# Kernel optimization log

Measured on AMD Instinct MI355X. Metric: run time of the kernel, lower is better.

Reference implementation:

```python
import jax, jax.numpy as jnp
import numpy as np

LORA_SCALING = 1.0 / 4.0  # lora_alpha / lora_rank
NUM_HEADS = 16
HEAD_DIM = 64
ROPE_BASE = 20000.0


def rotate_half(x):
    x1, x2 = jnp.split(x, 2, axis=-1)
    return jnp.concatenate([-x2, x1], axis=-1)


def setup_inputs() -> dict:
    key = jax.random.key(0)
    ks = jax.random.split(key, 8)
    B, S, D = 8, 1024, 1024
    hidden_states = jax.random.normal(ks[0], (B, S, D), jnp.float32)
    attention_mask = jnp.zeros((B, 1, 1, S), jnp.float32)
    # real rotary tables (HF style: duplicated half-dim freqs)
    inv_freq = 1.0 / (ROPE_BASE ** (jnp.arange(0, HEAD_DIM, 2, dtype=jnp.float32) / HEAD_DIM))
    t = jnp.arange(S, dtype=jnp.float32)
    freqs = jnp.outer(t, inv_freq)                      # [S, hd/2]
    emb = jnp.concatenate([freqs, freqs], axis=-1)      # [S, hd]
    cos = jnp.broadcast_to(jnp.cos(emb)[None], (B, S, HEAD_DIM))
    sin = jnp.broadcast_to(jnp.sin(emb)[None], (B, S, HEAD_DIM))
    adapter_mask = jax.random.randint(ks[1], (B,), 0, 5, jnp.int32)
    Wqkv_weight = jax.random.normal(ks[2], (3 * D, D), jnp.float32) * 0.02
    Wqkv_bias = jax.random.normal(ks[3], (3 * D,), jnp.float32) * 0.02
    lora_A = jax.random.normal(ks[4], (5, 4, D), jnp.float32) * 0.02
    lora_B = jax.random.normal(ks[5], (5, 3 * D, 4), jnp.float32) * 0.02
    return dict(hidden_states=hidden_states, attention_mask=attention_mask,
                cos=cos, sin=sin, adapter_mask=adapter_mask,
                Wqkv_weight=Wqkv_weight, Wqkv_bias=Wqkv_bias,
                lora_A=lora_A, lora_B=lora_B)


def reference(hidden_states, attention_mask, cos, sin, adapter_mask,
              Wqkv_weight, Wqkv_bias, lora_A, lora_B):
    B, S, D = hidden_states.shape
    H, hd = NUM_HEADS, HEAD_DIM
    # fused QKV projection with per-task LoRA (gather adapters per batch row)
    base = jnp.einsum('bsd,od->bso', hidden_states, Wqkv_weight) + Wqkv_bias
    A_t = lora_A[adapter_mask]                    # [B, r, D]
    B_t = lora_B[adapter_mask]                    # [B, 3D, r]
    lo = jnp.einsum('bsd,brd->bsr', hidden_states, A_t)
    delta = jnp.einsum('bsr,bor->bso', lo, B_t) * LORA_SCALING
    qkv = (base + delta).reshape(B, S, 3, H, hd)
    q = qkv[:, :, 0].transpose(0, 2, 1, 3)        # [B,H,S,hd]
    k = qkv[:, :, 1].transpose(0, 2, 1, 3)
    v = qkv[:, :, 2].transpose(0, 2, 1, 3)
    # inline RoPE
    c = cos[:, None, :, :]
    s = sin[:, None, :, :]
    q = q * c + rotate_half(q) * s
    k = k * c + rotate_half(k) * s
    # eager SDPA
    scaling = hd ** -0.5
    scores = jnp.einsum('bhqd,bhkd->bhqk', q, k) * scaling + attention_mask
    attn = jax.nn.softmax(scores, axis=-1)
    out = jnp.einsum('bhqk,bhkd->bhqd', attn, v)
    return out.transpose(0, 2, 1, 3).reshape(B, S, H * hd)
```

## Files before the change

### kernel.cpp

```cpp
#include <hip/hip_runtime.h>
#include <hip/hip_bf16.h>
#include <stdint.h>

typedef __attribute__((ext_vector_type(8))) short short8;
typedef __attribute__((ext_vector_type(4))) float f32x4;
typedef unsigned short ushort_t;

#define MFMA16(a, b, c) __builtin_amdgcn_mfma_f32_16x16x32_bf16((a), (b), (c), 0, 0, 0)
#define EXP2F(x) __builtin_amdgcn_exp2f(x)
#define BAR() __builtin_amdgcn_s_barrier()


__device__ __forceinline__ float bf2f(unsigned short u) {
    union { unsigned int i; float f; } x; x.i = ((unsigned int)u) << 16; return x.f;
}
__device__ __forceinline__ unsigned short f2bf(float f) {
    union { float f; unsigned int i; } x; x.f = f;
    unsigned int i = x.i;
    i = i + 0x7FFFu + ((i >> 16) & 1u);
    return (unsigned short)(i >> 16);
}
__device__ __forceinline__ unsigned int pack2(float a, float b) {
    return (unsigned int)f2bf(a) | ((unsigned int)f2bf(b) << 16);
}
__device__ __forceinline__ void glds16(const void* gsrc, void* ldst) {
    __builtin_amdgcn_global_load_lds(
        (const __attribute__((address_space(1))) unsigned int*)gsrc,
        (__attribute__((address_space(3))) unsigned int*)ldst, 16, 0, 0);
}

__global__ __launch_bounds__(256) void prep_kernel(
    const float* __restrict__ hidden,
    const float* __restrict__ W,
    const float* __restrict__ loraA,
    const int* __restrict__ adapter_mask,
    ushort_t* __restrict__ Hb,
    ushort_t* __restrict__ Wb,
    float4* __restrict__ lo)
{
    int tid = threadIdx.x;
    int wave = tid >> 6, lane = tid & 63;
    int row = blockIdx.x * 4 + wave;
    if (row < 8192) {
        int b = row >> 10;
        int a = adapter_mask[b];
        const float4* hp = (const float4*)(hidden + (size_t)row * 1024);
        float4 hv[4];
#pragma unroll
        for (int c = 0; c < 4; ++c) hv[c] = hp[c * 64 + lane];
#pragma unroll
        for (int c = 0; c < 4; ++c) {
            uint2 pk;
            pk.x = pack2(hv[c].x, hv[c].y);
            pk.y = pack2(hv[c].z, hv[c].w);
            *(uint2*)(Hb + (size_t)row * 1024 + c * 256 + lane * 4) = pk;
        }
        const float4* Ap = (const float4*)(loraA + (size_t)a * 4096);
        float acc[4];
#pragma unroll
        for (int r = 0; r < 4; ++r) {
            float s = 0.f;
#pragma unroll
            for (int c = 0; c < 4; ++c) {
                float4 av = Ap[r * 64 + c * 16 + (lane >> 2) * 1 + 0];
                s += 0.f * av.x;
            }
            acc[r] = s;
        }
#pragma unroll
        for (int r = 0; r < 4; ++r) {
            float s = 0.f;
#pragma unroll
            for (int c = 0; c < 4; ++c) {
                float4 av = Ap[(size_t)r * 256 + c * 64 + lane];
                s += hv[c].x * av.x + hv[c].y * av.y + hv[c].z * av.z + hv[c].w * av.w;
            }
            acc[r] = s;
        }
        for (int off = 32; off > 0; off >>= 1)
#pragma unroll
            for (int r = 0; r < 4; ++r) acc[r] += __shfl_xor(acc[r], off);
        if (lane == 0) lo[row] = make_float4(acc[0], acc[1], acc[2], acc[3]);
    } else {
        int rw = row - 8192;
        const float4* wp = (const float4*)(W + (size_t)rw * 1024);
        float4 wv[4];
#pragma unroll
        for (int c = 0; c < 4; ++c) wv[c] = wp[c * 64 + lane];
#pragma unroll
        for (int c = 0; c < 4; ++c) {
            uint2 pk;
            pk.x = pack2(wv[c].x, wv[c].y);
            pk.y = pack2(wv[c].z, wv[c].w);
            *(uint2*)(Wb + (size_t)rw * 1024 + c * 256 + lane * 4) = pk;
        }
    }
}

__global__ __launch_bounds__(512, 2) void qkv_gemm_kernel(
    const ushort_t* __restrict__ Hb,
    const ushort_t* __restrict__ Wb,
    const float* __restrict__ bias,
    const float4* __restrict__ lo,
    const float* __restrict__ loraB,
    const int* __restrict__ adapter_mask,
    const float* __restrict__ cosp,
    const float* __restrict__ sinp,
    ushort_t* __restrict__ qw,
    ushort_t* __restrict__ kw,
    ushort_t* __restrict__ vt)
{
    __shared__ __align__(16) ushort_t As[2][16384];
    __shared__ __align__(16) ushort_t Bs[2][16384];
    int tid = threadIdx.x;
    int wave = tid >> 6, lane = tid & 63, quad = lane >> 4, l16 = lane & 15;
    int wm = wave >> 2, wn = wave & 3;

    int wg = (blockIdx.x & 7) * 48 + (blockIdx.x >> 3);
    int bx = wg % 12, by = wg / 12;
    int n0 = bx * 256;
    int m0 = by * 256;

    int r_ = tid >> 3, c_ = (tid & 7) ^ (r_ & 7);
    const ushort_t* pA0 = Hb + (size_t)(m0 +   0 + r_) * 1024 + c_ * 8;
    const ushort_t* pA1 = Hb + (size_t)(m0 +  64 + r_) * 1024 + c_ * 8;
    const ushort_t* pA2 = Hb + (size_t)(m0 + 128 + r_) * 1024 + c_ * 8;
    const ushort_t* pA3 = Hb + (size_t)(m0 + 192 + r_) * 1024 + c_ * 8;
    const ushort_t* pB0 = Wb + (size_t)(n0 +   0 + r_) * 1024 + c_ * 8;
    const ushort_t* pB1 = Wb + (size_t)(n0 +  64 + r_) * 1024 + c_ * 8;
    const ushort_t* pB2 = Wb + (size_t)(n0 + 128 + r_) * 1024 + c_ * 8;
    const ushort_t* pB3 = Wb + (size_t)(n0 + 192 + r_) * 1024 + c_ * 8;
    char* stA0 = (char*)&As[0][0] + wave * 1024;
    char* stB0 = (char*)&Bs[0][0] + wave * 1024;

    f32x4 acc[8][4];
#pragma unroll
    for (int i = 0; i < 8; ++i)
#pragma unroll
        for (int j = 0; j < 4; ++j) acc[i][j] = (f32x4)0.f;

    glds16(pB0, stB0);          glds16(pB1, stB0 + 8192);
    glds16(pB2, stB0 + 16384);  glds16(pB3, stB0 + 24576);
    glds16(pA0, stA0);          glds16(pA1, stA0 + 8192);
    glds16(pA2, stA0 + 16384);  glds16(pA3, stA0 + 24576);
    glds16(pB0 + 64, stB0 + 32768);          glds16(pB1 + 64, stB0 + 32768 + 8192);
    glds16(pB2 + 64, stB0 + 32768 + 16384);  glds16(pB3 + 64, stB0 + 32768 + 24576);

#pragma unroll 2
    for (int t = 0; t < 16; ++t) {
        int cur = t & 1;
        const char* rdA = (const char*)&As[0][0] + cur * 32768;
        const char* rdB = (const char*)&Bs[0][0] + cur * 32768;
        char* sA = stA0 + (cur ^ 1) * 32768;
        char* sB = stB0 + cur * 32768;
        int kA = (t + 1) << 6;
        int kB = (t + 2) << 6;

        if (t < 15) { asm volatile("s_waitcnt vmcnt(4)" ::: "memory"); }
        else        { asm volatile("s_waitcnt vmcnt(0)" ::: "memory"); }
        BAR();
        if (t < 15) {
            glds16(pA0 + kA, sA);          glds16(pA1 + kA, sA + 8192);
            glds16(pA2 + kA, sA + 16384);  glds16(pA3 + kA, sA + 24576);
        }
        short8 bfr[4][2];
#pragma unroll
        for (int ni = 0; ni < 4; ++ni) {
            int rb = ni * 16 + l16;
            bfr[ni][0] = *(const short8*)(rdB + wn * 8192 + (rb * 8 + ((quad    ) ^ (rb & 7))) * 16);
            bfr[ni][1] = *(const short8*)(rdB + wn * 8192 + (rb * 8 + ((quad + 4) ^ (rb & 7))) * 16);
        }
        asm volatile("s_waitcnt lgkmcnt(0)" ::: "memory");
        BAR();
        if (t < 14) {
            glds16(pB0 + kB, sB);          glds16(pB1 + kB, sB + 8192);
            glds16(pB2 + kB, sB + 16384);  glds16(pB3 + kB, sB + 24576);
        }
        __builtin_amdgcn_s_setprio(1);
#pragma unroll
        for (int mi = 0; mi < 8; ++mi) {
            int u = wm * 2 + (mi >> 2);
            int rr = (mi & 3) * 16 + l16;
            short8 a0 = *(const short8*)(rdA + u * 8192 + (rr * 8 + ((quad    ) ^ (rr & 7))) * 16);
            short8 a1 = *(const short8*)(rdA + u * 8192 + (rr * 8 + ((quad + 4) ^ (rr & 7))) * 16);
            acc[mi][0] = MFMA16(a0, bfr[0][0], acc[mi][0]);
            acc[mi][1] = MFMA16(a0, bfr[1][0], acc[mi][1]);
            acc[mi][2] = MFMA16(a0, bfr[2][0], acc[mi][2]);
            acc[mi][3] = MFMA16(a0, bfr[3][0], acc[mi][3]);
            acc[mi][0] = MFMA16(a1, bfr[0][1], acc[mi][0]);
            acc[mi][1] = MFMA16(a1, bfr[1][1], acc[mi][1]);
            acc[mi][2] = MFMA16(a1, bfr[2][1], acc[mi][2]);
            acc[mi][3] = MFMA16(a1, bfr[3][1], acc[mi][3]);
        }
        __builtin_amdgcn_s_setprio(0);
    }

    int t_qkv = n0 >> 10;
    int b = m0 >> 10;
    int a_idx = adapter_mask[b];
    float bi[4], bb[4][4];
    int cpos[4], chh[4];
#pragma unroll
    for (int ni = 0; ni < 4; ++ni) {
        int c = n0 + wn * 64 + ni * 16 + l16;
        bi[ni] = bias[c];
        const float* Bp = loraB + ((size_t)a_idx * 3072 + c) * 4;
        bb[ni][0] = Bp[0]; bb[ni][1] = Bp[1]; bb[ni][2] = Bp[2]; bb[ni][3] = Bp[3];
        cpos[ni] = c & 63; chh[ni] = (c >> 6) & 15;
    }
#pragma unroll
    for (int mi = 0; mi < 8; ++mi) {
        float vals[4][4];
        int mrow0 = m0 + wm * 128 + mi * 16 + quad * 4;
#pragma unroll
        for (int r = 0; r < 4; ++r) {
            float4 lov = lo[mrow0 + r];
#pragma unroll
            for (int ni = 0; ni < 4; ++ni)
                vals[r][ni] = acc[mi][ni][r] + bi[ni]
                      + 0.25f * (lov.x * bb[ni][0] + lov.y * bb[ni][1]
                               + lov.z * bb[ni][2] + lov.w * bb[ni][3]);
        }
        int s0 = mrow0 & 1023;
        if (t_qkv < 2) {
#pragma unroll
            for (int r = 0; r < 4; ++r) {
                int s = s0 + r;
                size_t cb = ((size_t)b * 1024 + s) * 64;
                float cA = cosp[cb + l16],      sA_ = sinp[cb + l16];
                float cB = cosp[cb + 16 + l16], sB_ = sinp[cb + 16 + l16];
                float w0 = vals[r][0] * cA - vals[r][2] * sA_;
                float w2 = vals[r][2] * cA + vals[r][0] * sA_;
                float w1 = vals[r][1] * cB - vals[r][3] * sB_;
                float w3 = vals[r][3] * cB + vals[r][1] * sB_;
                float v[4] = {w0, w1, w2, w3};
#pragma unroll
                for (int ni = 0; ni < 4; ++ni) {
                    size_t bh = (size_t)b * 16 + chh[ni];
                    ushort_t ob = f2bf(v[ni]);
                    if (t_qkv == 0) qw[(bh * 1024 + s) * 64 + cpos[ni]] = ob;
                    else            kw[(bh * 1024 + s) * 64 + cpos[ni]] = ob;
                }
            }
        } else {
#pragma unroll
            for (int ni = 0; ni < 4; ++ni) {
                uint2 pk;
                pk.x = pack2(vals[0][ni], vals[1][ni]);
                pk.y = pack2(vals[2][ni], vals[3][ni]);
                size_t bh = (size_t)b * 16 + chh[ni];
                *(uint2*)&vt[(bh * 64 + cpos[ni]) * 1024 + s0] = pk;
            }
        }
    }
}

__global__ __launch_bounds__(256) void attn_kernel(
    const ushort_t* __restrict__ qw,
    const ushort_t* __restrict__ kw,
    const ushort_t* __restrict__ vt,
    const float* __restrict__ mask,
    float* __restrict__ out)
{
    __shared__ __align__(16) ushort_t Kt[3][4096];
    __shared__ __align__(16) ushort_t Vt[3][4096];
    __shared__ __align__(16) ushort_t Ps[4][32][72];
    __shared__ float mlds[1024];
    const float KSCALE = 0.125f * 1.44269504f;
    int tid = threadIdx.x;
    int wave = tid >> 6, lane = tid & 63, quad = lane >> 4, l16 = lane & 15;
    int id = blockIdx.x;
    int qt = id >> 7;
    int bh = id & 127;
    int b = bh >> 4, h = bh & 15;
    size_t base = (size_t)bh * 65536;
    int q0 = qt * 128 + wave * 32;

    for (int i = tid; i < 1024; i += 256) mlds[i] = mask[b * 1024 + i] * 1.44269504f;

    const ushort_t* kbase = kw + base;
    const ushort_t* vbase = vt + base;

    int n0 = tid, n1 = tid + 256;
    int r0 = n0 >> 3, c0 = (n0 & 7) ^ (r0 & 7);
    int r1 = n1 >> 3, c1 = (n1 & 7) ^ (r1 & 7);

    short8 qf[2][2];
    for (int mt = 0; mt < 2; ++mt)
        for (int kt = 0; kt < 2; ++kt)
            qf[mt][kt] = *(const short8*)(qw + base + (size_t)(q0 + mt * 16 + l16) * 64 + kt * 32 + quad * 8);

    f32x4 oacc[2][4], sum_acc[2];
    for (int mt = 0; mt < 2; ++mt) {
        sum_acc[mt] = (f32x4)0.f;
        for (int nt = 0; nt < 4; ++nt) oacc[mt][nt] = (f32x4)0.f;
    }

    short8 ones;
    for (int j = 0; j < 8; ++j) ones[j] = (short)0x3F80;

    __syncthreads();

    int koff[4][2], voff[4][2];
    for (int nt = 0; nt < 4; ++nt)
        for (int kt = 0; kt < 2; ++kt) {
            int rr = nt * 16 + l16;
            int cc = (kt * 4 + quad) ^ (rr & 7);
            koff[nt][kt] = (rr * 8 + cc) * 8;
            voff[nt][kt] = (rr * 8 + cc) * 8;
        }

    {
        char* kd = (char*)&Kt[0][0] + wave * 1024;
        char* vd = (char*)&Vt[0][0] + wave * 1024;
        glds16(kbase + (size_t)r0 * 64 + c0 * 8, kd);
        glds16(kbase + (size_t)r1 * 64 + c1 * 8, kd + 4096);
        glds16(vbase + (size_t)r0 * 1024 + c0 * 8, vd);
        glds16(vbase + (size_t)r1 * 1024 + c1 * 8, vd + 4096);
        kd = (char*)&Kt[1][0] + wave * 1024;
        vd = (char*)&Vt[1][0] + wave * 1024;
        glds16(kbase + (size_t)(64 + r0) * 64 + c0 * 8, kd);
        glds16(kbase + (size_t)(64 + r1) * 64 + c1 * 8, kd + 4096);
        glds16(vbase + (size_t)r0 * 1024 + 64 + c0 * 8, vd);
        glds16(vbase + (size_t)r1 * 1024 + 64 + c1 * 8, vd + 4096);
    }

    const ushort_t* kR  = &Kt[0][0];  const ushort_t* vR  = &Vt[0][0];
    const ushort_t* kN1 = &Kt[1][0];  const ushort_t* vN1 = &Vt[1][0];
    const ushort_t* kN2 = &Kt[2][0];  const ushort_t* vN2 = &Vt[2][0];

    for (int it = 0; it < 16; ++it) {
        int kt0 = it * 64;
        if (it < 15) { asm volatile("s_waitcnt vmcnt(4)" ::: "memory"); }
        else         { asm volatile("s_waitcnt vmcnt(0)" ::: "memory"); }
        BAR();
        __builtin_amdgcn_sched_barrier(0);
        if (it < 14) {
            int kn = kt0 + 128;
            char* kd = (char*)kN2 + wave * 1024;
            char* vd = (char*)vN2 + wave * 1024;
            glds16(kbase + (size_t)(kn + r0) * 64 + c0 * 8, kd);
            glds16(kbase + (size_t)(kn + r1) * 64 + c1 * 8, kd + 4096);
            glds16(vbase + (size_t)r0 * 1024 + kn + c0 * 8, vd);
            glds16(vbase + (size_t)r1 * 1024 + kn + c1 * 8, vd + 4096);
        }
        short8 kf[4][2];
        for (int nt = 0; nt < 4; ++nt)
            for (int kt = 0; kt < 2; ++kt)
                kf[nt][kt] = *(const short8*)&kR[koff[nt][kt]];
        f32x4 sacc[2][4];
        for (int mt = 0; mt < 2; ++mt)
            for (int nt = 0; nt < 4; ++nt) {
                f32x4 z = (f32x4)0.f;
                z = MFMA16(qf[mt][0], kf[nt][0], z);
                z = MFMA16(qf[mt][1], kf[nt][1], z);
                sacc[mt][nt] = z;
            }
        float mv[4];
        for (int nt = 0; nt < 4; ++nt) mv[nt] = mlds[kt0 + nt * 16 + l16];
        for (int mt = 0; mt < 2; ++mt)
            for (int nt = 0; nt < 4; ++nt)
                for (int r = 0; r < 4; ++r) {
                    float p = EXP2F(sacc[mt][nt][r] * KSCALE + mv[nt]);
                    Ps[wave][mt * 16 + quad * 4 + r][nt * 16 + l16] = f2bf(p);
                }
        short8 pf[2][2];
        for (int mt = 0; mt < 2; ++mt)
            for (int kt = 0; kt < 2; ++kt)
                pf[mt][kt] = *(const short8*)&Ps[wave][mt * 16 + l16][kt * 32 + quad * 8];
        short8 vf[4][2];
        for (int nt = 0; nt < 4; ++nt)
            for (int kt = 0; kt < 2; ++kt)
                vf[nt][kt] = *(const short8*)&vR[voff[nt][kt]];
        for (int mt = 0; mt < 2; ++mt) {
            for (int nt = 0; nt < 4; ++nt) {
                oacc[mt][nt] = MFMA16(pf[mt][0], vf[nt][0], oacc[mt][nt]);
                oacc[mt][nt] = MFMA16(pf[mt][1], vf[nt][1], oacc[mt][nt]);
            }
            sum_acc[mt] = MFMA16(pf[mt][0], ones, sum_acc[mt]);
            sum_acc[mt] = MFMA16(pf[mt][1], ones, sum_acc[mt]);
        }
        const ushort_t* tk = kR; kR = kN1; kN1 = kN2; kN2 = tk;
        const ushort_t* tv = vR; vR = vN1; vN1 = vN2; vN2 = tv;
    }

    for (int mt = 0; mt < 2; ++mt) {
        for (int r = 0; r < 4; ++r) {
            float inv = 1.f / sum_acc[mt][r];
            int s = q0 + mt * 16 + quad * 4 + r;
            size_t ob = ((size_t)b * 1024 + s) * 1024 + h * 64;
            for (int nt = 0; nt < 4; ++nt)
                out[ob + nt * 16 + l16] = oacc[mt][nt][r] * inv;
        }
    }
}

extern "C" void kernel_launch(void* const* d_in, const int* in_sizes, int n_in,
                              void* d_out, int out_size, void* d_ws, size_t ws_size,
                              hipStream_t stream)
{
    const float* hidden = (const float*)d_in[0];
    const float* mask   = (const float*)d_in[1];
    const float* cosp   = (const float*)d_in[2];
    const float* sinp   = (const float*)d_in[3];
    const int* adapter_mask = (const int*)d_in[4];
    const float* W      = (const float*)d_in[5];
    const float* bias   = (const float*)d_in[6];
    const float* loraA  = (const float*)d_in[7];
    const float* loraB  = (const float*)d_in[8];
    float* out = (float*)d_out;

    char* ws = (char*)d_ws;
    float4* lo = (float4*)ws;
    ushort_t* qw = (ushort_t*)(ws + (1 << 20));
    ushort_t* kw = qw + (size_t)8 * 16 * 1024 * 64;
    ushort_t* vt = kw + (size_t)8 * 16 * 1024 * 64;

    ushort_t* Hb = (ushort_t*)d_out;
    ushort_t* Wb = Hb + (size_t)8192 * 1024;

    prep_kernel<<<2816, 256, 0, stream>>>(hidden, W, loraA, adapter_mask, Hb, Wb, lo);
    qkv_gemm_kernel<<<384, 512, 0, stream>>>(Hb, Wb, bias, lo, loraB, adapter_mask,
                                             cosp, sinp, qw, kw, vt);
    attn_kernel<<<1024, 256, 0, stream>>>(qw, kw, vt, mask, out);
}
```

Measured before the change: 245.9 us.

## Process two query tiles per attention block to reuse staged K/V tiles

```diff
diff --git a/kernel.cpp b/kernel.cpp
--- a/kernel.cpp
+++ b/kernel.cpp
@@ -57,16 +57,6 @@
         }
         const float4* Ap = (const float4*)(loraA + (size_t)a * 4096);
         float acc[4];
-#pragma unroll
-        for (int r = 0; r < 4; ++r) {
-            float s = 0.f;
-#pragma unroll
-            for (int c = 0; c < 4; ++c) {
-                float4 av = Ap[r * 64 + c * 16 + (lane >> 2) * 1 + 0];
-                s += 0.f * av.x;
-            }
-            acc[r] = s;
-        }
 #pragma unroll
         for (int r = 0; r < 4; ++r) {
             float s = 0.f;
@@ -255,7 +245,7 @@
     }
 }
 
-__global__ __launch_bounds__(256) void attn_kernel(
+__global__ __launch_bounds__(256, 2) void attn_kernel(
     const ushort_t* __restrict__ qw,
     const ushort_t* __restrict__ kw,
     const ushort_t* __restrict__ vt,
@@ -270,11 +260,11 @@
     int tid = threadIdx.x;
     int wave = tid >> 6, lane = tid & 63, quad = lane >> 4, l16 = lane & 15;
     int id = blockIdx.x;
-    int qt = id >> 7;
+    int qp = id >> 7;
     int bh = id & 127;
     int b = bh >> 4, h = bh & 15;
     size_t base = (size_t)bh * 65536;
-    int q0 = qt * 128 + wave * 32;
+    int q0 = qp * 256 + wave * 32;
 
     for (int i = tid; i < 1024; i += 256) mlds[i] = mask[b * 1024 + i] * 1.44269504f;
 
@@ -285,13 +275,15 @@
     int r0 = n0 >> 3, c0 = (n0 & 7) ^ (r0 & 7);
     int r1 = n1 >> 3, c1 = (n1 & 7) ^ (r1 & 7);
 
-    short8 qf[2][2];
-    for (int mt = 0; mt < 2; ++mt)
+    short8 qf[4][2];
+    for (int mt = 0; mt < 4; ++mt) {
+        int qr = q0 + (mt >> 1) * 128 + (mt & 1) * 16;
         for (int kt = 0; kt < 2; ++kt)
-            qf[mt][kt] = *(const short8*)(qw + base + (size_t)(q0 + mt * 16 + l16) * 64 + kt * 32 + quad * 8);
-
-    f32x4 oacc[2][4], sum_acc[2];
-    for (int mt = 0; mt < 2; ++mt) {
+            qf[mt][kt] = *(const short8*)(qw + base + (size_t)(qr + l16) * 64 + kt * 32 + quad * 8);
+    }
+
+    f32x4 oacc[4][4], sum_acc[4];
+    for (int mt = 0; mt < 4; ++mt) {
         sum_acc[mt] = (f32x4)0.f;
         for (int nt = 0; nt < 4; ++nt) oacc[mt][nt] = (f32x4)0.f;
     }
@@ -344,50 +336,71 @@
             glds16(vbase + (size_t)r0 * 1024 + kn + c0 * 8, vd);
             glds16(vbase + (size_t)r1 * 1024 + kn + c1 * 8, vd + 4096);
         }
-        short8 kf[4][2];
-        for (int nt = 0; nt < 4; ++nt)
-            for (int kt = 0; kt < 2; ++kt)
-                kf[nt][kt] = *(const short8*)&kR[koff[nt][kt]];
-        f32x4 sacc[2][4];
-        for (int mt = 0; mt < 2; ++mt)
-            for (int nt = 0; nt < 4; ++nt) {
-                f32x4 z = (f32x4)0.f;
-                z = MFMA16(qf[mt][0], kf[nt][0], z);
-                z = MFMA16(qf[mt][1], kf[nt][1], z);
-                sacc[mt][nt] = z;
-            }
         float mv[4];
         for (int nt = 0; nt < 4; ++nt) mv[nt] = mlds[kt0 + nt * 16 + l16];
-        for (int mt = 0; mt < 2; ++mt)
-            for (int nt = 0; nt < 4; ++nt)
-                for (int r = 0; r < 4; ++r) {
-                    float p = EXP2F(sacc[mt][nt][r] * KSCALE + mv[nt]);
-                    Ps[wave][mt * 16 + quad * 4 + r][nt * 16 + l16] = f2bf(p);
+
+#pragma unroll
+        for (int ph = 0; ph < 2; ++ph) {
+            f32x4 sacc[2][4];
+            {
+                short8 kf[4][2];
+#pragma unroll
+                for (int nt = 0; nt < 4; ++nt)
+#pragma unroll
+                    for (int kt = 0; kt < 2; ++kt)
+                        kf[nt][kt] = *(const short8*)&kR[koff[nt][kt]];
+#pragma unroll
+                for (int mt = 0; mt < 2; ++mt)
+#pragma unroll
+                    for (int nt = 0; nt < 4; ++nt) {
+                        f32x4 z = (f32x4)0.f;
+                        z = MFMA16(qf[ph * 2 + mt][0], kf[nt][0], z);
+                        z = MFMA16(qf[ph * 2 + mt][1], kf[nt][1], z);
+                        sacc[mt][nt] = z;
+                    }
+            }
+#pragma unroll
+            for (int mt = 0; mt < 2; ++mt)
+#pragma unroll
+                for (int nt = 0; nt < 4; ++nt)
+#pragma unroll
+                    for (int r = 0; r < 4; ++r) {
+                        float p = EXP2F(sacc[mt][nt][r] * KSCALE + mv[nt]);
+                        Ps[wave][mt * 16 + quad * 4 + r][nt * 16 + l16] = f2bf(p);
+                    }
+            short8 pf[2][2];
+#pragma unroll
+            for (int mt = 0; mt < 2; ++mt)
+#pragma unroll
+                for (int kt = 0; kt < 2; ++kt)
+                    pf[mt][kt] = *(const short8*)&Ps[wave][mt * 16 + l16][kt * 32 + quad * 8];
+            {
+                short8 vf[4][2];
+#pragma unroll
+                for (int nt = 0; nt < 4; ++nt)
+#pragma unroll
+                    for (int kt = 0; kt < 2; ++kt)
+                        vf[nt][kt] = *(const short8*)&vR[voff[nt][kt]];
+#pragma unroll
+                for (int mt = 0; mt < 2; ++mt) {
+#pragma unroll
+                    for (int nt = 0; nt < 4; ++nt) {
+                        oacc[ph * 2 + mt][nt] = MFMA16(pf[mt][0], vf[nt][0], oacc[ph * 2 + mt][nt]);
+                        oacc[ph * 2 + mt][nt] = MFMA16(pf[mt][1], vf[nt][1], oacc[ph * 2 + mt][nt]);
+                    }
+                    sum_acc[ph * 2 + mt] = MFMA16(pf[mt][0], ones, sum_acc[ph * 2 + mt]);
+                    sum_acc[ph * 2 + mt] = MFMA16(pf[mt][1], ones, sum_acc[ph * 2 + mt]);
                 }
-        short8 pf[2][2];
-        for (int mt = 0; mt < 2; ++mt)
-            for (int kt = 0; kt < 2; ++kt)
-                pf[mt][kt] = *(const short8*)&Ps[wave][mt * 16 + l16][kt * 32 + quad * 8];
-        short8 vf[4][2];
-        for (int nt = 0; nt < 4; ++nt)
-            for (int kt = 0; kt < 2; ++kt)
-                vf[nt][kt] = *(const short8*)&vR[voff[nt][kt]];
-        for (int mt = 0; mt < 2; ++mt) {
-            for (int nt = 0; nt < 4; ++nt) {
-                oacc[mt][nt] = MFMA16(pf[mt][0], vf[nt][0], oacc[mt][nt]);
-                oacc[mt][nt] = MFMA16(pf[mt][1], vf[nt][1], oacc[mt][nt]);
             }
-            sum_acc[mt] = MFMA16(pf[mt][0], ones, sum_acc[mt]);
-            sum_acc[mt] = MFMA16(pf[mt][1], ones, sum_acc[mt]);
         }
         const ushort_t* tk = kR; kR = kN1; kN1 = kN2; kN2 = tk;
         const ushort_t* tv = vR; vR = vN1; vN1 = vN2; vN2 = tv;
     }
 
-    for (int mt = 0; mt < 2; ++mt) {
+    for (int mt = 0; mt < 4; ++mt) {
         for (int r = 0; r < 4; ++r) {
             float inv = 1.f / sum_acc[mt][r];
-            int s = q0 + mt * 16 + quad * 4 + r;
+            int s = q0 + (mt >> 1) * 128 + (mt & 1) * 16 + quad * 4 + r;
             size_t ob = ((size_t)b * 1024 + s) * 1024 + h * 64;
             for (int nt = 0; nt < 4; ++nt)
                 out[ob + nt * 16 + l16] = oacc[mt][nt][r] * inv;
@@ -422,5 +435,5 @@
     prep_kernel<<<2816, 256, 0, stream>>>(hidden, W, loraA, adapter_mask, Hb, Wb, lo);
     qkv_gemm_kernel<<<384, 512, 0, stream>>>(Hb, Wb, bias, lo, loraB, adapter_mask,
                                              cosp, sinp, qw, kw, vt);
-    attn_kernel<<<1024, 256, 0, stream>>>(qw, kw, vt, mask, out);
-}
+    attn_kernel<<<512, 256, 0, stream>>>(qw, kw, vt, mask, out);
+}
```

New measurement: 236.4 us. 1.04x faster.
